# Kernel optimization log

Measured on AMD Instinct MI355X. Metric: run time of the kernel, lower is better.

## Reference

```python
import jax, jax.numpy as jnp
import numpy as np

N_NODES = 20000
N_EDGES = 320000
N_GRAPHS = 200
N_LAYERS = 2
TOWERS = 5
F_IN = 75        # divide_input=False -> each tower sees the full 75-dim input
F_OUT = 15       # out_channels // towers = 75 // 5
EDGE_DIM = 50
POST_IN = (4 * 3 + 1) * F_IN  # 4 aggregators * 3 scalers + self = 975
EPS_STD = 1e-5
EPS_BN = 1e-5


def setup_inputs() -> dict:
    key = jax.random.key(0)
    ks = jax.random.split(key, 16)
    x_idx = jax.random.randint(ks[0], (N_NODES,), 0, 10000)
    edge_index = jax.random.randint(ks[1], (2, N_EDGES), 0, N_NODES)
    edge_attr_idx = jax.random.randint(ks[2], (N_EDGES,), 0, 100)
    batch_idx = jnp.sort(jax.random.randint(ks[3], (N_NODES,), 0, N_GRAPHS))

    def g(k, shp, fan):
        return jax.random.normal(k, shp, jnp.float32) * np.float32(1.0 / np.sqrt(fan))

    inp = dict(
        x_idx=x_idx, edge_index=edge_index, edge_attr_idx=edge_attr_idx, batch_idx=batch_idx,
        node_emb=g(ks[4], (10000, F_IN), 1.0),
        edge_emb=g(ks[5], (100, EDGE_DIM), 1.0),
        W_edge=g(ks[6], (N_LAYERS, EDGE_DIM, F_IN), EDGE_DIM),
        b_edge=jnp.zeros((N_LAYERS, F_IN), jnp.float32),
        W_pre=g(ks[7], (N_LAYERS, TOWERS, 3 * F_IN, F_IN), 3 * F_IN),
        b_pre=jnp.zeros((N_LAYERS, TOWERS, F_IN), jnp.float32),
        W_post=g(ks[8], (N_LAYERS, TOWERS, POST_IN, F_OUT), POST_IN),
        b_post=jnp.zeros((N_LAYERS, TOWERS, F_OUT), jnp.float32),
        W_lin=g(ks[9], (N_LAYERS, F_IN, F_IN), F_IN),
        b_lin=jnp.zeros((N_LAYERS, F_IN), jnp.float32),
        bn_gamma=jnp.ones((N_LAYERS, F_IN), jnp.float32),
        bn_beta=jnp.zeros((N_LAYERS, F_IN), jnp.float32),
        W1=g(ks[10], (75, 50), 75), b1=jnp.zeros((50,), jnp.float32),
        W2=g(ks[11], (50, 25), 50), b2=jnp.zeros((25,), jnp.float32),
        W3=g(ks[12], (25, 1), 25), b3=jnp.zeros((1,), jnp.float32),
    )
    return inp


def reference(x_idx, edge_index, edge_attr_idx, batch_idx,
              node_emb, edge_emb, W_edge, b_edge, W_pre, b_pre,
              W_post, b_post, W_lin, b_lin, bn_gamma, bn_beta,
              W1, b1, W2, b2, W3, b3):
    src, dst = edge_index[0], edge_index[1]  # flow source_to_target: aggregate at dst
    x = node_emb[x_idx]                      # [N, 75]
    e_raw = edge_emb[edge_attr_idx]          # [E, 50]

    # in-degree based scalers (PNA); avg log-degree from this graph's degree histogram
    deg = jax.ops.segment_sum(jnp.ones((N_EDGES,), jnp.float32), dst, num_segments=N_NODES)
    avg_log = jnp.mean(jnp.log(deg + 1.0))
    deg_c = jnp.maximum(deg, 1.0)
    amp = (jnp.log(deg_c + 1.0) / avg_log)[:, None, None]
    att = (avg_log / jnp.log(deg_c + 1.0))[:, None, None]
    has_in = (deg > 0.0)[:, None, None]
    inv_deg = (1.0 / deg_c)[:, None, None]

    for l in range(N_LAYERS):
        # edge encoder (shared across towers)
        e = e_raw @ W_edge[l] + b_edge[l]                            # [E, 75]
        # message: since divide_input=False all towers see the same concat input
        h = jnp.concatenate([x[dst], x[src], e], axis=-1)            # [E, 225]
        m = jnp.einsum('ec,tcf->etf', h, W_pre[l]) + b_pre[l]        # [E, T, 75]
        # multi-aggregator reduction at dst
        mean = jax.ops.segment_sum(m, dst, num_segments=N_NODES) * inv_deg
        mean_sq = jax.ops.segment_sum(m * m, dst, num_segments=N_NODES) * inv_deg
        std = jnp.sqrt(jax.nn.relu(mean_sq - mean * mean) + EPS_STD)
        mn = jnp.where(has_in, jax.ops.segment_min(m, dst, num_segments=N_NODES), 0.0)
        mx = jnp.where(has_in, jax.ops.segment_max(m, dst, num_segments=N_NODES), 0.0)
        aggr = jnp.concatenate([mean, mn, mx, std], axis=-1)         # [N, T, 300]
        # degree scalers: identity, amplification, attenuation
        out = jnp.concatenate([aggr, aggr * amp, aggr * att], axis=-1)  # [N, T, 900]
        # update: concat self features, per-tower post MLP, then shared lin
        xt = jnp.broadcast_to(x[:, None, :], (N_NODES, TOWERS, F_IN))
        h2 = jnp.concatenate([xt, out], axis=-1)                     # [N, T, 975]
        y = jnp.einsum('ntc,tcf->ntf', h2, W_post[l]) + b_post[l]    # [N, T, 15]
        y = y.reshape(N_NODES, TOWERS * F_OUT) @ W_lin[l] + b_lin[l] # [N, 75]
        # BatchNorm (training-mode batch stats, biased variance) + ReLU
        mu = jnp.mean(y, axis=0)
        var = jnp.mean((y - mu) ** 2, axis=0)
        y = (y - mu) * jax.lax.rsqrt(var + EPS_BN) * bn_gamma[l] + bn_beta[l]
        x = jax.nn.relu(y)

    pooled = jax.ops.segment_sum(x, batch_idx, num_segments=N_GRAPHS)  # [G, 75]
    h = jax.nn.relu(pooled @ W1 + b1)
    h = jax.nn.relu(h @ W2 + b2)
    return h @ W3 + b3                                               # [G, 1]
```

## Files before the change

kernel.cpp:

```cpp
#include <hip/hip_runtime.h>
#include <hip/hip_bf16.h>
#include <math.h>

#define NN 20000
#define NE 320000
#define NG 200
#define FI 75
#define NT 5
#define FO 15
#define CH 375
#define PI 975

typedef __attribute__((ext_vector_type(8))) short v8s;
typedef __attribute__((ext_vector_type(4))) float v4f;

__device__ __forceinline__ unsigned short f2bfu(float v) {
  __hip_bfloat16 h = __float2bfloat16(v);
  return *reinterpret_cast<unsigned short*>(&h);
}
__device__ __forceinline__ float uif(unsigned u) { return __uint_as_float(u); }

__global__ __launch_bounds__(256) void k_mega1(
    const int* __restrict__ xidx, const float* __restrict__ emb, float* __restrict__ x,
    const int* __restrict__ dstp, int* __restrict__ deg,
    const float* __restrict__ eemb, const float* __restrict__ W_edge,
    const float* __restrict__ b_edge, float* __restrict__ te,
    const float* __restrict__ W_pre, float* __restrict__ WAs,
    const float* __restrict__ W_post, float* __restrict__ V,
    const float* __restrict__ b_post, const float* __restrict__ W_lin,
    const float* __restrict__ b_lin, float* __restrict__ bc) {
  __shared__ float S[FI * 16];
  int b = blockIdx.x, tid = threadIdx.x;
  if (b < 5860) {
    int i = b * 256 + tid;
    if (i < NN * FI) {
      int n = i / FI, f = i - n * FI;
      x[i] = emb[xidx[n] * FI + f];
    }
  } else if (b < 7110) {
    int e = (b - 5860) * 256 + tid;
    if (e < NE) atomicAdd(&deg[dstp[e]], 1);
  } else if (b < 7310) {
    int la = b - 7110;
    int l = la / 100, a = la - l * 100;
    int f = tid;
    if (f < FI) {
      float acc = b_edge[l * FI + f];
      for (int j = 0; j < 50; ++j)
        acc = fmaf(eemb[a * 50 + j], W_edge[(l * 50 + j) * FI + f], acc);
      te[la * FI + f] = acc;
    }
  } else if (b < 7530) {
    int i = (b - 7310) * 256 + tid;
    if (i < 2 * FI * CH) {
      int c = i % CH;
      int k = (i / CH) % FI;
      int l = i / (CH * FI);
      int t = c / FI, f = c - t * FI;
      WAs[i] = W_pre[((size_t)(l * NT + t) * 225 + FI + k) * FI + f];
    }
  } else if (b < 7560) {
    int bid = b - 7530;
    int g = bid % 3;
    int lt = bid / 3;
    for (int idx = tid; idx < FI * 16; idx += 256) {
      int q = idx >> 4, f = idx & 15;
      float v = 0.f;
      if (f < FO) {
        const float* wb = W_post + (size_t)lt * PI * FO;
        int rowb = FI + g * 300 + q;
        v = wb[rowb * FO + f] + wb[(rowb + FI) * FO + f] + wb[(rowb + 2 * FI) * FO + f];
      }
      S[idx] = v;
    }
    __syncthreads();
    for (int idx = tid; idx < FI * 16; idx += 256) {
      int j = idx >> 4, f = idx & 15;
      float acc = 0.f;
      const float* wr = W_pre + ((size_t)lt * 225 + j) * FI;
      for (int q = 0; q < FI; ++q) acc = fmaf(wr[q], S[q * 16 + f], acc);
      V[((size_t)bid * FI + j) * 16 + f] = acc;
    }
  } else {
    int l = b - 7560;
    int g = tid;
    if (g < FI) {
      float acc = b_lin[l * FI + g];
      for (int j = 0; j < FI; ++j)
        acc = fmaf(b_post[l * FI + j], W_lin[(l * FI + j) * FI + g], acc);
      bc[l * 76 + g] = acc;
    }
  }
}

__global__ __launch_bounds__(1024) void k_mega2(
    const int* __restrict__ deg, int* __restrict__ off, int* __restrict__ cur,
    float* __restrict__ avglog,
    const float* __restrict__ te, const float* __restrict__ W_pre,
    const float* __restrict__ b_pre, unsigned short* __restrict__ tm,
    const float* __restrict__ W_post, const float* __restrict__ V,
    unsigned short* __restrict__ Bp,
    const float* __restrict__ WAs, unsigned short* __restrict__ Bxs) {
  __shared__ float red[1024];
  int b = blockIdx.x, t = threadIdx.x;
  if (b == 0) {
    int* wsum = (int*)red;
    int base = t * 20;
    int loc[20];
    int s = 0;
#pragma unroll
    for (int j = 0; j < 20; ++j) {
      int i = base + j;
      int v = (i < NN) ? deg[i] : 0;
      loc[j] = s;
      s += v;
    }
    int lane = t & 63, w = t >> 6;
    int inc = s;
    for (int o = 1; o < 64; o <<= 1) {
      int u = __shfl_up(inc, o, 64);
      if (lane >= o) inc += u;
    }
    if (lane == 63) wsum[w] = inc;
    __syncthreads();
    if (t == 0) {
      int a = 0;
#pragma unroll
      for (int k = 0; k < 16; ++k) { int v = wsum[k]; wsum[k] = a; a += v; }
    }
    __syncthreads();
    int tex = wsum[w] + inc - s;
#pragma unroll
    for (int j = 0; j < 20; ++j) {
      int i = base + j;
      if (i < NN) { int e = tex + loc[j]; off[i] = e; cur[i] = e; }
    }
    if (t == 1023) off[NN] = tex + s;
  } else if (b == 1) {
    float s = 0.f;
    for (int i = t; i < NN; i += 1024) s += logf((float)deg[i] + 1.f);
    red[t] = s;
    __syncthreads();
    for (int o = 512; o > 0; o >>= 1) {
      if (t < o) red[t] += red[t + o];
      __syncthreads();
    }
    if (t == 0) avglog[0] = red[0] / (float)NN;
  } else if (b < 77) {
    int idx = (b - 2) * 1024 + t;
    if (idx < 76800) {
      int la = idx / 384, c = idx - la * 384;
      int l = la / 100;
      float acc = 0.f;
      if (c < CH) {
        int tt = c / FI, f = c - tt * FI;
        acc = b_pre[(l * NT + tt) * FI + f];
        const float* ter = te + la * FI;
        for (int k = 0; k < FI; ++k)
          acc = fmaf(ter[k], W_pre[((size_t)(l * NT + tt) * 225 + 150 + k) * FI + f], acc);
      }
      tm[(size_t)la * 384 + c] = f2bfu(acc);
    }
  } else if (b < 302) {
    int i = (b - 77) * 1024 + t;
    if (i < 230400) {
      int j = i & 7;
      int lane = (i >> 3) & 63;
      int rem = i >> 9;
      int kb = rem % 15; rem /= 15;
      int g = rem % 3; rem /= 3;
      int tt = rem % 5;
      int l = rem / 5;
      int k = kb * 32 + (lane >> 4) * 8 + j;
      int f = lane & 15;
      float w = 0.f;
      if (f < FO) {
        int lt = l * NT + tt;
        if (k < 300) {
          int a = k / 75, ch = k - a * 75;
          w = W_post[((size_t)lt * PI + FI + g * 300 + a * 75 + ch) * FO + f];
        } else if (k >= 320 && k < 395) {
          w = V[(((size_t)(lt * 3 + g)) * FI + (k - 320)) * 16 + f];
        } else if (k >= 395 && k < 470 && g == 0) {
          w = W_post[((size_t)lt * PI + (k - 395)) * FO + f];
        }
      }
      Bp[i] = f2bfu(w);
    }
  } else {
    int i = (b - 302) * 1024 + t;
    if (i < 73728) {
      int j = i & 7;
      int lane = (i >> 3) & 63;
      int rem = i >> 9;
      int nt = rem % 24; rem /= 24;
      int kb = rem % 3;
      int l = rem / 3;
      int k = kb * 32 + (lane >> 4) * 8 + j;
      int n = nt * 16 + (lane & 15);
      float w = 0.f;
      if (k < FI && n < CH) w = WAs[(size_t)l * FI * CH + k * CH + n];
      Bxs[i] = f2bfu(w);
    }
  }
}

__global__ __launch_bounds__(256) void k_mega3(
    const int* __restrict__ srcp, const int* __restrict__ dstp,
    const int* __restrict__ attr, int* __restrict__ cur, int2* __restrict__ csr,
    const int* __restrict__ deg, const float* __restrict__ avglog,
    float* __restrict__ amp, float* __restrict__ att, float* __restrict__ inv) {
  int b = blockIdx.x, t = threadIdx.x;
  if (b < 1250) {
    int e = b * 256 + t;
    if (e < NE) {
      int pos = atomicAdd(&cur[dstp[e]], 1);
      csr[pos] = make_int2(srcp[e], attr[e]);
    }
  } else {
    int i = (b - 1250) * 256 + t;
    if (i < NN) {
      float dc = fmaxf((float)deg[i], 1.f);
      float ld = logf(dc + 1.f);
      float av = avglog[0];
      amp[i] = ld / av;
      att[i] = av / ld;
      inv[i] = 1.f / dc;
    }
  }
}

__global__ __launch_bounds__(256) void k_gemm_xs(const float* __restrict__ x,
                                                 const unsigned short* __restrict__ BxsL,
                                                 unsigned short* __restrict__ xsb,
                                                 const int* __restrict__ deg,
                                                 unsigned short* __restrict__ xh,
                                                 float* __restrict__ bnsum) {
  int tid = threadIdx.x;
  if (blockIdx.y == 1) {
    if (blockIdx.x == 0 && tid < 150) bnsum[tid] = 0.f;
    for (int i = blockIdx.x * 256 + tid; i < NN * 160; i += 625 * 256) {
      int r = i / 160, k = i - r * 160;
      float v = 0.f;
      if (k < FI) v = x[(size_t)r * FI + k] * ((deg[r] > 0) ? 1.f : 0.f);
      else if (k < 150) v = x[(size_t)r * FI + k - FI];
      xh[i] = f2bfu(v);
    }
    return;
  }
  __shared__ unsigned short As[32 * 104];
  __shared__ unsigned short Os[32 * 384];
  int m0 = blockIdx.x * 32;
  for (int i = tid; i < 32 * 104; i += 256) {
    int r = i / 104, k = i - r * 104;
    As[i] = (k < FI) ? f2bfu(x[(size_t)(m0 + r) * FI + k]) : 0;
  }
  __syncthreads();
  int lane = tid & 63, w = tid >> 6;
  int m16 = lane & 15, quad = lane >> 4;
  v4f acc0[6], acc1[6];
#pragma unroll
  for (int nt = 0; nt < 6; ++nt) {
    acc0[nt] = {0.f, 0.f, 0.f, 0.f};
    acc1[nt] = {0.f, 0.f, 0.f, 0.f};
  }
  const unsigned short* arow0 = As + m16 * 104 + quad * 8;
  const unsigned short* arow1 = As + (16 + m16) * 104 + quad * 8;
#pragma unroll
  for (int kb = 0; kb < 3; ++kb) {
    v8s a0 = *(const v8s*)(arow0 + kb * 32);
    v8s a1 = *(const v8s*)(arow1 + kb * 32);
#pragma unroll
    for (int nt = 0; nt < 6; ++nt) {
      v8s bf = *(const v8s*)(BxsL + ((size_t)(kb * 24 + w * 6 + nt) * 64 + lane) * 8);
      acc0[nt] = __builtin_amdgcn_mfma_f32_16x16x32_bf16(a0, bf, acc0[nt], 0, 0, 0);
      acc1[nt] = __builtin_amdgcn_mfma_f32_16x16x32_bf16(a1, bf, acc1[nt], 0, 0, 0);
    }
  }
#pragma unroll
  for (int nt = 0; nt < 6; ++nt) {
    int col = w * 96 + nt * 16 + m16;
#pragma unroll
    for (int r = 0; r < 4; ++r) {
      Os[(quad * 4 + r) * 384 + col] = f2bfu(acc0[nt][r]);
      Os[(16 + quad * 4 + r) * 384 + col] = f2bfu(acc1[nt][r]);
    }
  }
  __syncthreads();
  uint4* dst = (uint4*)(xsb + (size_t)m0 * 384);
  const uint4* src = (const uint4*)Os;
  for (int i = tid; i < 1536; i += 256) dst[i] = src[i];
}

__global__ __launch_bounds__(192) void k_aggregate(int n0, int cn,
    const unsigned short* __restrict__ xs, const int2* __restrict__ csr,
    const int* __restrict__ off, const float* __restrict__ inv_deg,
    const unsigned short* __restrict__ tm, unsigned short* __restrict__ aggA) {
  __shared__ unsigned short sm[4 * 1600];
  int tid = threadIdx.x;
  int sub = tid / 48;
  int lane48 = tid - sub * 48;
  int rel0 = blockIdx.x * 4;
  int rel = rel0 + sub;
  for (int idx = tid; idx < 400; idx += 192) {
    int h = idx / 100, pp = idx - h * 100;
    int t = pp / 20, cc = pp - t * 20;
    sm[h * 1600 + t * 320 + 300 + cc] = 0;
  }
  if (rel < cn) {
    int n = n0 + rel;
    int c0 = lane48 * 8;
    int o0 = off[n], o1 = off[n + 1];
    float s[8], q[8], mn[8], mx[8];
#pragma unroll
    for (int j = 0; j < 8; ++j) {
      s[j] = 0.f; q[j] = 0.f; mn[j] = INFINITY; mx[j] = -INFINITY;
    }
    auto proc = [&](uint4 xv, uint4 tv) {
      unsigned xa[4] = {xv.x, xv.y, xv.z, xv.w};
      unsigned ta[4] = {tv.x, tv.y, tv.z, tv.w};
#pragma unroll
      for (int j = 0; j < 4; ++j) {
        float z0 = uif(xa[j] << 16) + uif(ta[j] << 16);
        float z1 = uif(xa[j] & 0xffff0000u) + uif(ta[j] & 0xffff0000u);
        s[2 * j] += z0; q[2 * j] = fmaf(z0, z0, q[2 * j]);
        mn[2 * j] = fminf(mn[2 * j], z0); mx[2 * j] = fmaxf(mx[2 * j], z0);
        s[2 * j + 1] += z1; q[2 * j + 1] = fmaf(z1, z1, q[2 * j + 1]);
        mn[2 * j + 1] = fminf(mn[2 * j + 1], z1); mx[2 * j + 1] = fmaxf(mx[2 * j + 1], z1);
      }
    };
    int i = o0;
    for (; i + 8 <= o1; i += 8) {
      int2 e0 = csr[i], e1 = csr[i + 1], e2 = csr[i + 2], e3 = csr[i + 3];
      int2 e4 = csr[i + 4], e5 = csr[i + 5], e6 = csr[i + 6], e7 = csr[i + 7];
      uint4 x0 = *(const uint4*)(xs + (size_t)e0.x * 384 + c0);
      uint4 t0 = *(const uint4*)(tm + (size_t)e0.y * 384 + c0);
      uint4 x1 = *(const uint4*)(xs + (size_t)e1.x * 384 + c0);
      uint4 t1 = *(const uint4*)(tm + (size_t)e1.y * 384 + c0);
      uint4 x2 = *(const uint4*)(xs + (size_t)e2.x * 384 + c0);
      uint4 t2 = *(const uint4*)(tm + (size_t)e2.y * 384 + c0);
      uint4 x3 = *(const uint4*)(xs + (size_t)e3.x * 384 + c0);
      uint4 t3 = *(const uint4*)(tm + (size_t)e3.y * 384 + c0);
      uint4 x4 = *(const uint4*)(xs + (size_t)e4.x * 384 + c0);
      uint4 t4 = *(const uint4*)(tm + (size_t)e4.y * 384 + c0);
      uint4 x5 = *(const uint4*)(xs + (size_t)e5.x * 384 + c0);
      uint4 t5 = *(const uint4*)(tm + (size_t)e5.y * 384 + c0);
      uint4 x6 = *(const uint4*)(xs + (size_t)e6.x * 384 + c0);
      uint4 t6 = *(const uint4*)(tm + (size_t)e6.y * 384 + c0);
      uint4 x7 = *(const uint4*)(xs + (size_t)e7.x * 384 + c0);
      uint4 t7 = *(const uint4*)(tm + (size_t)e7.y * 384 + c0);
      proc(x0, t0); proc(x1, t1); proc(x2, t2); proc(x3, t3);
      proc(x4, t4); proc(x5, t5); proc(x6, t6); proc(x7, t7);
    }
    for (; i + 2 <= o1; i += 2) {
      int2 e0 = csr[i], e1 = csr[i + 1];
      uint4 x0 = *(const uint4*)(xs + (size_t)e0.x * 384 + c0);
      uint4 t0 = *(const uint4*)(tm + (size_t)e0.y * 384 + c0);
      uint4 x1 = *(const uint4*)(xs + (size_t)e1.x * 384 + c0);
      uint4 t1 = *(const uint4*)(tm + (size_t)e1.y * 384 + c0);
      proc(x0, t0); proc(x1, t1);
    }
    if (i < o1) {
      int2 e0 = csr[i];
      uint4 x0 = *(const uint4*)(xs + (size_t)e0.x * 384 + c0);
      uint4 t0 = *(const uint4*)(tm + (size_t)e0.y * 384 + c0);
      proc(x0, t0);
    }
    float inv = inv_deg[n];
    bool empty = (o1 == o0);
    unsigned short* srow = sm + sub * 1600;
#pragma unroll
    for (int j = 0; j < 8; ++j) {
      int c = c0 + j;
      if (c < CH) {
        float me = s[j] * inv;
        float sd = sqrtf(fmaxf(q[j] * inv - me * me, 0.f) + 1e-5f);
        float mnv = empty ? 0.f : mn[j];
        float mxv = empty ? 0.f : mx[j];
        int t = c / 75, ch = c - t * 75;
        unsigned short* bb = srow + t * 320;
        bb[ch] = f2bfu(me);
        bb[75 + ch] = f2bfu(mnv);
        bb[150 + ch] = f2bfu(mxv);
        bb[225 + ch] = f2bfu(sd);
      }
    }
  }
  __syncthreads();
  int nrow = cn - rel0;
  if (nrow > 4) nrow = 4;
  if (nrow > 0) {
    int nu4 = nrow * 200;
    uint4* dst = (uint4*)(aggA + (size_t)rel0 * 1600);
    const uint4* src = (const uint4*)sm;
    for (int idx = tid; idx < nu4; idx += 192) dst[idx] = src[idx];
  }
}

__global__ __launch_bounds__(128) void k_mfma_post(int n0, int nend,
    const unsigned short* __restrict__ aggA, const unsigned short* __restrict__ xh,
    const unsigned short* __restrict__ Bp, const float* __restrict__ amp,
    const float* __restrict__ att, float* __restrict__ z) {
  int t = blockIdx.y;
  int lane = threadIdx.x & 63;
  int wv = threadIdx.x >> 6;
  int m16 = lane & 15, quad = lane >> 4;
  int relA = blockIdx.x * 32 + wv * 16 + m16;
  const unsigned short* arow = aggA + (size_t)relA * 1600 + t * 320 + quad * 8;
  const unsigned short* xrow = xh + (size_t)(n0 + relA) * 160 + quad * 8;
  const unsigned short* bp = Bp + ((size_t)t * 3 * 15 * 64) * 8 + lane * 8;
  v4f a0 = {0.f, 0.f, 0.f, 0.f}, a1 = a0, a2 = a0;
#pragma unroll
  for (int kb = 0; kb < 15; ++kb) {
    v8s av = *(const v8s*)((kb < 10) ? (arow + kb * 32) : (xrow + (kb - 10) * 32));
    const unsigned short* bb = bp + (size_t)kb * 512;
    v8s b0 = *(const v8s*)(bb);
    v8s b1 = *(const v8s*)(bb + 15 * 512);
    v8s b2 = *(const v8s*)(bb + 30 * 512);
    a0 = __builtin_amdgcn_mfma_f32_16x16x32_bf16(av, b0, a0, 0, 0, 0);
    a1 = __builtin_amdgcn_mfma_f32_16x16x32_bf16(av, b1, a1, 0, 0, 0);
    a2 = __builtin_amdgcn_mfma_f32_16x16x32_bf16(av, b2, a2, 0, 0, 0);
  }
  int f = m16;
  if (f < FO) {
    int relD0 = blockIdx.x * 32 + wv * 16 + quad * 4;
#pragma unroll
    for (int r = 0; r < 4; ++r) {
      int nd = n0 + relD0 + r;
      if (nd < nend) {
        float zz = a0[r] + amp[nd] * a1[r] + att[nd] * a2[r];
        z[(size_t)nd * FI + t * FO + f] = zz;
      }
    }
  }
}

__global__ __launch_bounds__(256) void k_gemm75(const float* __restrict__ zin,
    const float* __restrict__ Wl, const float* __restrict__ bcL,
    float* __restrict__ yout, float* __restrict__ bnsum) {
  __shared__ float Zs[64 * FI];
  __shared__ float Ws[FI * 76];
  __shared__ float ysum[FI], ysq[FI];
  int tid = threadIdx.x;
  int n0 = blockIdx.x * 64;
  for (int i = tid; i < 64 * FI; i += 256) {
    int n = n0 + i / FI;
    Zs[i] = (n < NN) ? zin[(size_t)n0 * FI + i] : 0.f;
  }
  for (int i = tid; i < FI * FI; i += 256) {
    int k = i / FI, f = i - k * FI;
    Ws[k * 76 + f] = Wl[i];
  }
  if (tid < FI) { ysum[tid] = 0.f; ysq[tid] = 0.f; }
  __syncthreads();
  int nl = tid >> 2, fg = tid & 3;
  int f0 = fg * 19;
  float acc[19];
#pragma unroll
  for (int i = 0; i < 19; ++i) acc[i] = bcL[f0 + i];
  for (int k = 0; k < FI; ++k) {
    float a = Zs[nl * FI + k];
#pragma unroll
    for (int i = 0; i < 19; ++i) acc[i] = fmaf(a, Ws[k * 76 + f0 + i], acc[i]);
  }
  int n = n0 + nl;
  if (n < NN) {
#pragma unroll
    for (int i = 0; i < 19; ++i) {
      int f = f0 + i;
      if (f < FI) {
        float v = acc[i];
        yout[(size_t)n * FI + f] = v;
        atomicAdd(&ysum[f], v);
        atomicAdd(&ysq[f], v * v);
      }
    }
  }
  __syncthreads();
  if (tid < FI) {
    atomicAdd(&bnsum[tid], ysum[tid]);
    atomicAdd(&bnsum[FI + tid], ysq[tid]);
  }
}

__global__ __launch_bounds__(256) void k_bnfinapply(const float* __restrict__ y,
    const float* __restrict__ bnsum, const float* __restrict__ gamL,
    const float* __restrict__ betL, float* __restrict__ xo,
    const int* __restrict__ batch, float* __restrict__ pooled, int dopool) {
  __shared__ float sc[150];
  int tid = threadIdx.x;
  if (tid < FI) {
    float mu = bnsum[tid] / (float)NN;
    float var = bnsum[FI + tid] / (float)NN - mu * mu;
    float scl = gamL[tid] * rsqrtf(var + 1e-5f);
    sc[tid] = scl;
    sc[FI + tid] = betL[tid] - mu * scl;
  }
  if (!dopool) {
    for (int i = blockIdx.x * 256 + tid; i < NG * FI; i += gridDim.x * 256)
      pooled[i] = 0.f;
  }
  __syncthreads();
  int stride = gridDim.x * 256;
  for (int i = blockIdx.x * 256 + tid; i < NN * FI; i += stride) {
    int n = i / FI, f = i - n * FI;
    float v = fmaxf(fmaf(y[i], sc[f], sc[FI + f]), 0.f);
    xo[i] = v;
    if (dopool) atomicAdd(&pooled[batch[n] * FI + f], v);
  }
}

__global__ void k_head(const float* __restrict__ pooled, const float* __restrict__ W1,
                       const float* __restrict__ b1, const float* __restrict__ W2,
                       const float* __restrict__ b2, const float* __restrict__ W3,
                       const float* __restrict__ b3, float* __restrict__ out) {
  __shared__ float p[FI], h1[50], h2[25];
  int g = blockIdx.x, t = threadIdx.x;
  for (int i = t; i < FI; i += 64) p[i] = pooled[g * FI + i];
  __syncthreads();
  if (t < 50) {
    float a = b1[t];
    for (int j = 0; j < FI; ++j) a = fmaf(p[j], W1[j * 50 + t], a);
    h1[t] = fmaxf(a, 0.f);
  }
  __syncthreads();
  if (t < 25) {
    float a = b2[t];
    for (int j = 0; j < 50; ++j) a = fmaf(h1[j], W2[j * 25 + t], a);
    h2[t] = fmaxf(a, 0.f);
  }
  __syncthreads();
  if (t == 0) {
    float a = b3[0];
    for (int j = 0; j < 25; ++j) a = fmaf(h2[j], W3[j], a);
    out[g] = a;
  }
}

extern "C" void kernel_launch(void* const* d_in, const int* in_sizes, int n_in,
                              void* d_out, int out_size, void* d_ws, size_t ws_size,
                              hipStream_t stream) {
  const int* x_idx = (const int*)d_in[0];
  const int* eidx  = (const int*)d_in[1];
  const int* srcp  = eidx;
  const int* dstp  = eidx + NE;
  const int* eattr = (const int*)d_in[2];
  const int* batch = (const int*)d_in[3];
  const float* node_emb = (const float*)d_in[4];
  const float* edge_emb = (const float*)d_in[5];
  const float* W_edge = (const float*)d_in[6];
  const float* b_edge = (const float*)d_in[7];
  const float* W_pre  = (const float*)d_in[8];
  const float* b_pre  = (const float*)d_in[9];
  const float* W_post = (const float*)d_in[10];
  const float* b_post = (const float*)d_in[11];
  const float* W_lin  = (const float*)d_in[12];
  const float* b_lin  = (const float*)d_in[13];
  const float* gam = (const float*)d_in[14];
  const float* bet = (const float*)d_in[15];
  const float* W1 = (const float*)d_in[16];
  const float* b1 = (const float*)d_in[17];
  const float* W2 = (const float*)d_in[18];
  const float* b2 = (const float*)d_in[19];
  const float* W3 = (const float*)d_in[20];
  const float* b3 = (const float*)d_in[21];

  char* p = (char*)d_ws;
  auto alloc = [&](size_t b) -> char* {
    char* r = p;
    p += (b + 255) & ~(size_t)255;
    return r;
  };
  float* x_a   = (float*)alloc((size_t)NN * FI * 4);
  float* x_b   = (float*)alloc((size_t)NN * FI * 4);
  unsigned short* xs_bf = (unsigned short*)alloc((size_t)NN * 384 * 2);
  float* z     = (float*)alloc((size_t)NN * FI * 4);
  unsigned short* xh = (unsigned short*)alloc((size_t)(NN + 32) * 160 * 2);
  float* te    = (float*)alloc(2 * 100 * FI * 4);
  unsigned short* tm_bf = (unsigned short*)alloc((size_t)2 * 100 * 384 * 2);
  float* WAs   = (float*)alloc((size_t)2 * FI * CH * 4);
  float* V     = (float*)alloc((size_t)2 * NT * 3 * FI * 16 * 4);
  unsigned short* Bpk = (unsigned short*)alloc((size_t)230400 * 2);
  unsigned short* Bxs = (unsigned short*)alloc((size_t)73728 * 2);
  float* bc    = (float*)alloc(2 * 76 * 4);
  float* ampv  = (float*)alloc((size_t)NN * 4);
  float* attv  = (float*)alloc((size_t)NN * 4);
  float* invv  = (float*)alloc((size_t)NN * 4);
  float* avglog = (float*)alloc(256);
  float* bnsum = (float*)alloc(2 * FI * 4);
  float* pooled = (float*)alloc((size_t)NG * FI * 4);
  int* deg = (int*)alloc((size_t)NN * 4);
  int* off = (int*)alloc((size_t)(NN + 1) * 4);
  int* cur = (int*)alloc((size_t)NN * 4);
  int2* csr = (int2*)alloc((size_t)NE * 8);
  size_t used = (size_t)(p - (char*)d_ws);
  int chunkN = NN;
  while (chunkN > 2500 &&
         used + (size_t)((chunkN + 31) & ~31) * 1600 * 2 + (1 << 20) > ws_size)
    chunkN >>= 1;
  int rows = (chunkN + 31) & ~31;
  unsigned short* aggA = (unsigned short*)alloc((size_t)rows * 1600 * 2);

  hipMemsetAsync(deg, 0, (size_t)NN * 4, stream);

  k_mega1<<<7562, 256, 0, stream>>>(x_idx, node_emb, x_a, dstp, deg,
                                    edge_emb, W_edge, b_edge, te,
                                    W_pre, WAs, W_post, V,
                                    b_post, W_lin, b_lin, bc);
  k_mega2<<<374, 1024, 0, stream>>>(deg, off, cur, avglog,
                                    te, W_pre, b_pre, tm_bf, W_post, V, Bpk,
                                    WAs, Bxs);
  k_mega3<<<1329, 256, 0, stream>>>(srcp, dstp, eattr, cur, csr,
                                    deg, avglog, ampv, attv, invv);

  for (int l = 0; l < 2; ++l) {
    const float* xin = (l == 0) ? x_a : x_b;
    float* xout = (l == 0) ? x_b : x_a;
    k_gemm_xs<<<dim3(625, 2), 256, 0, stream>>>(xin, Bxs + (size_t)l * 36864,
                                                xs_bf, deg, xh, bnsum);
    for (int n0 = 0; n0 < NN; n0 += chunkN) {
      int cn = (NN - n0 < chunkN) ? (NN - n0) : chunkN;
      k_aggregate<<<(cn + 3) / 4, 192, 0, stream>>>(n0, cn, xs_bf, csr, off, invv,
                                                    tm_bf + (size_t)l * 100 * 384, aggA);
      k_mfma_post<<<dim3((cn + 31) / 32, 5), 128, 0, stream>>>(
          n0, n0 + cn, aggA, xh, Bpk + (size_t)l * 115200, ampv, attv, z);
    }
    k_gemm75<<<313, 256, 0, stream>>>(z, W_lin + (size_t)l * FI * FI, bc + l * 76,
                                      z, bnsum);
    k_bnfinapply<<<1250, 256, 0, stream>>>(z, bnsum, gam + l * FI, bet + l * FI,
                                           xout, batch, pooled, (l == 1) ? 1 : 0);
  }

  k_head<<<NG, 64, 0, stream>>>(pooled, W1, b1, W2, b2, W3, b3, (float*)d_out);
}
```

Measured before the change: 490.8 us.

## Process nodes in descending-degree order via counting-sort permutation for load balance

```diff
diff --git a/kernel.cpp b/kernel.cpp
--- a/kernel.cpp
+++ b/kernel.cpp
@@ -28,7 +28,8 @@
     const float* __restrict__ W_pre, float* __restrict__ WAs,
     const float* __restrict__ W_post, float* __restrict__ V,
     const float* __restrict__ b_post, const float* __restrict__ W_lin,
-    const float* __restrict__ b_lin, float* __restrict__ bc) {
+    const float* __restrict__ b_lin, float* __restrict__ bc,
+    int* __restrict__ hist) {
   __shared__ float S[FI * 16];
   int b = blockIdx.x, tid = threadIdx.x;
   if (b < 5860) {
@@ -81,7 +82,7 @@
       for (int q = 0; q < FI; ++q) acc = fmaf(wr[q], S[q * 16 + f], acc);
       V[((size_t)bid * FI + j) * 16 + f] = acc;
     }
-  } else {
+  } else if (b < 7562) {
     int l = b - 7560;
     int g = tid;
     if (g < FI) {
@@ -90,6 +91,8 @@
         acc = fmaf(b_post[l * FI + j], W_lin[(l * FI + j) * FI + g], acc);
       bc[l * 76 + g] = acc;
     }
+  } else {
+    for (int i = tid; i < 1024; i += 256) hist[i] = 0;
   }
 }
 
@@ -100,7 +103,8 @@
     const float* __restrict__ b_pre, unsigned short* __restrict__ tm,
     const float* __restrict__ W_post, const float* __restrict__ V,
     unsigned short* __restrict__ Bp,
-    const float* __restrict__ WAs, unsigned short* __restrict__ Bxs) {
+    const float* __restrict__ WAs, unsigned short* __restrict__ Bxs,
+    int* __restrict__ hist) {
   __shared__ float red[1024];
   int b = blockIdx.x, t = threadIdx.x;
   if (b == 0) {
@@ -187,7 +191,7 @@
       }
       Bp[i] = f2bfu(w);
     }
-  } else {
+  } else if (b < 374) {
     int i = (b - 302) * 1024 + t;
     if (i < 73728) {
       int j = i & 7;
@@ -202,6 +206,43 @@
       if (k < FI && n < CH) w = WAs[(size_t)l * FI * CH + k * CH + n];
       Bxs[i] = f2bfu(w);
     }
+  } else {
+    int i = (b - 374) * 1024 + t;
+    if (i < NN) {
+      int d = deg[i];
+      if (d > 1023) d = 1023;
+      atomicAdd(&hist[1023 - d], 1);
+    }
+  }
+}
+
+__global__ __launch_bounds__(1024) void k_scanperm(const int* __restrict__ deg,
+                                                   int* __restrict__ hist,
+                                                   int* __restrict__ perm) {
+  __shared__ int ws[16];
+  int t = threadIdx.x;
+  int v = hist[t];
+  int lane = t & 63, w = t >> 6;
+  int inc = v;
+  for (int o = 1; o < 64; o <<= 1) {
+    int u = __shfl_up(inc, o, 64);
+    if (lane >= o) inc += u;
+  }
+  if (lane == 63) ws[w] = inc;
+  __syncthreads();
+  if (t == 0) {
+    int a = 0;
+#pragma unroll
+    for (int k = 0; k < 16; ++k) { int x = ws[k]; ws[k] = a; a += x; }
+  }
+  __syncthreads();
+  hist[t] = ws[w] + inc - v;
+  __syncthreads();
+  for (int n = t; n < NN; n += 1024) {
+    int d = deg[n];
+    if (d > 1023) d = 1023;
+    int pos = atomicAdd(&hist[1023 - d], 1);
+    perm[pos] = n;
   }
 }
 
@@ -295,7 +336,8 @@
 __global__ __launch_bounds__(192) void k_aggregate(int n0, int cn,
     const unsigned short* __restrict__ xs, const int2* __restrict__ csr,
     const int* __restrict__ off, const float* __restrict__ inv_deg,
-    const unsigned short* __restrict__ tm, unsigned short* __restrict__ aggA) {
+    const unsigned short* __restrict__ tm, unsigned short* __restrict__ aggA,
+    const int* __restrict__ perm) {
   __shared__ unsigned short sm[4 * 1600];
   int tid = threadIdx.x;
   int sub = tid / 48;
@@ -308,7 +350,7 @@
     sm[h * 1600 + t * 320 + 300 + cc] = 0;
   }
   if (rel < cn) {
-    int n = n0 + rel;
+    int n = perm[n0 + rel];
     int c0 = lane48 * 8;
     int o0 = off[n], o1 = off[n + 1];
     float s[8], q[8], mn[8], mx[8];
@@ -400,14 +442,18 @@
 __global__ __launch_bounds__(128) void k_mfma_post(int n0, int nend,
     const unsigned short* __restrict__ aggA, const unsigned short* __restrict__ xh,
     const unsigned short* __restrict__ Bp, const float* __restrict__ amp,
-    const float* __restrict__ att, float* __restrict__ z) {
+    const float* __restrict__ att, float* __restrict__ z,
+    const int* __restrict__ perm) {
   int t = blockIdx.y;
   int lane = threadIdx.x & 63;
   int wv = threadIdx.x >> 6;
   int m16 = lane & 15, quad = lane >> 4;
   int relA = blockIdx.x * 32 + wv * 16 + m16;
+  int idxA = n0 + relA;
+  if (idxA >= NN) idxA = NN - 1;
+  int ndA = perm[idxA];
   const unsigned short* arow = aggA + (size_t)relA * 1600 + t * 320 + quad * 8;
-  const unsigned short* xrow = xh + (size_t)(n0 + relA) * 160 + quad * 8;
+  const unsigned short* xrow = xh + (size_t)ndA * 160 + quad * 8;
   const unsigned short* bp = Bp + ((size_t)t * 3 * 15 * 64) * 8 + lane * 8;
   v4f a0 = {0.f, 0.f, 0.f, 0.f}, a1 = a0, a2 = a0;
 #pragma unroll
@@ -426,8 +472,9 @@
     int relD0 = blockIdx.x * 32 + wv * 16 + quad * 4;
 #pragma unroll
     for (int r = 0; r < 4; ++r) {
-      int nd = n0 + relD0 + r;
-      if (nd < nend) {
+      int slot = n0 + relD0 + r;
+      if (slot < nend) {
+        int nd = perm[slot];
         float zz = a0[r] + amp[nd] * a1[r] + att[nd] * a2[r];
         z[(size_t)nd * FI + t * FO + f] = zz;
       }
@@ -592,6 +639,8 @@
   int* deg = (int*)alloc((size_t)NN * 4);
   int* off = (int*)alloc((size_t)(NN + 1) * 4);
   int* cur = (int*)alloc((size_t)NN * 4);
+  int* hist = (int*)alloc(1024 * 4);
+  int* perm = (int*)alloc((size_t)NN * 4);
   int2* csr = (int2*)alloc((size_t)NE * 8);
   size_t used = (size_t)(p - (char*)d_ws);
   int chunkN = NN;
@@ -603,13 +652,14 @@
 
   hipMemsetAsync(deg, 0, (size_t)NN * 4, stream);
 
-  k_mega1<<<7562, 256, 0, stream>>>(x_idx, node_emb, x_a, dstp, deg,
+  k_mega1<<<7563, 256, 0, stream>>>(x_idx, node_emb, x_a, dstp, deg,
                                     edge_emb, W_edge, b_edge, te,
                                     W_pre, WAs, W_post, V,
-                                    b_post, W_lin, b_lin, bc);
-  k_mega2<<<374, 1024, 0, stream>>>(deg, off, cur, avglog,
+                                    b_post, W_lin, b_lin, bc, hist);
+  k_mega2<<<394, 1024, 0, stream>>>(deg, off, cur, avglog,
                                     te, W_pre, b_pre, tm_bf, W_post, V, Bpk,
-                                    WAs, Bxs);
+                                    WAs, Bxs, hist);
+  k_scanperm<<<1, 1024, 0, stream>>>(deg, hist, perm);
   k_mega3<<<1329, 256, 0, stream>>>(srcp, dstp, eattr, cur, csr,
                                     deg, avglog, ampv, attv, invv);
 
@@ -621,9 +671,10 @@
     for (int n0 = 0; n0 < NN; n0 += chunkN) {
       int cn = (NN - n0 < chunkN) ? (NN - n0) : chunkN;
       k_aggregate<<<(cn + 3) / 4, 192, 0, stream>>>(n0, cn, xs_bf, csr, off, invv,
-                                                    tm_bf + (size_t)l * 100 * 384, aggA);
+                                                    tm_bf + (size_t)l * 100 * 384, aggA,
+                                                    perm);
       k_mfma_post<<<dim3((cn + 31) / 32, 5), 128, 0, stream>>>(
-          n0, n0 + cn, aggA, xh, Bpk + (size_t)l * 115200, ampv, attv, z);
+          n0, n0 + cn, aggA, xh, Bpk + (size_t)l * 115200, ampv, attv, z, perm);
     }
     k_gemm75<<<313, 256, 0, stream>>>(z, W_lin + (size_t)l * FI * FI, bc + l * 76,
                                       z, bnsum);
```

Measured after the change: 648.1 us. 32.0% more time.

## Fuse per-tower MFMA post projection with shared 75x75 linear and BN stats

Applied to the files above, without the earlier changes.

```diff
diff --git a/kernel.cpp b/kernel.cpp
--- a/kernel.cpp
+++ b/kernel.cpp
@@ -397,74 +397,67 @@
   }
 }
 
-__global__ __launch_bounds__(128) void k_mfma_post(int n0, int nend,
+__global__ __launch_bounds__(128) void k_post2(int n0, int nend,
     const unsigned short* __restrict__ aggA, const unsigned short* __restrict__ xh,
     const unsigned short* __restrict__ Bp, const float* __restrict__ amp,
-    const float* __restrict__ att, float* __restrict__ z) {
-  int t = blockIdx.y;
-  int lane = threadIdx.x & 63;
-  int wv = threadIdx.x >> 6;
-  int m16 = lane & 15, quad = lane >> 4;
-  int relA = blockIdx.x * 32 + wv * 16 + m16;
-  const unsigned short* arow = aggA + (size_t)relA * 1600 + t * 320 + quad * 8;
-  const unsigned short* xrow = xh + (size_t)(n0 + relA) * 160 + quad * 8;
-  const unsigned short* bp = Bp + ((size_t)t * 3 * 15 * 64) * 8 + lane * 8;
-  v4f a0 = {0.f, 0.f, 0.f, 0.f}, a1 = a0, a2 = a0;
-#pragma unroll
-  for (int kb = 0; kb < 15; ++kb) {
-    v8s av = *(const v8s*)((kb < 10) ? (arow + kb * 32) : (xrow + (kb - 10) * 32));
-    const unsigned short* bb = bp + (size_t)kb * 512;
-    v8s b0 = *(const v8s*)(bb);
-    v8s b1 = *(const v8s*)(bb + 15 * 512);
-    v8s b2 = *(const v8s*)(bb + 30 * 512);
-    a0 = __builtin_amdgcn_mfma_f32_16x16x32_bf16(av, b0, a0, 0, 0, 0);
-    a1 = __builtin_amdgcn_mfma_f32_16x16x32_bf16(av, b1, a1, 0, 0, 0);
-    a2 = __builtin_amdgcn_mfma_f32_16x16x32_bf16(av, b2, a2, 0, 0, 0);
-  }
-  int f = m16;
-  if (f < FO) {
-    int relD0 = blockIdx.x * 32 + wv * 16 + quad * 4;
-#pragma unroll
-    for (int r = 0; r < 4; ++r) {
-      int nd = n0 + relD0 + r;
-      if (nd < nend) {
-        float zz = a0[r] + amp[nd] * a1[r] + att[nd] * a2[r];
-        z[(size_t)nd * FI + t * FO + f] = zz;
-      }
-    }
-  }
-}
-
-__global__ __launch_bounds__(256) void k_gemm75(const float* __restrict__ zin,
-    const float* __restrict__ Wl, const float* __restrict__ bcL,
-    float* __restrict__ yout, float* __restrict__ bnsum) {
-  __shared__ float Zs[64 * FI];
+    const float* __restrict__ att, const float* __restrict__ Wl,
+    const float* __restrict__ bcL, float* __restrict__ yout,
+    float* __restrict__ bnsum) {
+  __shared__ float zs[32][76];
   __shared__ float Ws[FI * 76];
   __shared__ float ysum[FI], ysq[FI];
   int tid = threadIdx.x;
-  int n0 = blockIdx.x * 64;
-  for (int i = tid; i < 64 * FI; i += 256) {
-    int n = n0 + i / FI;
-    Zs[i] = (n < NN) ? zin[(size_t)n0 * FI + i] : 0.f;
-  }
-  for (int i = tid; i < FI * FI; i += 256) {
+  for (int i = tid; i < FI * FI; i += 128) {
     int k = i / FI, f = i - k * FI;
     Ws[k * 76 + f] = Wl[i];
   }
   if (tid < FI) { ysum[tid] = 0.f; ysq[tid] = 0.f; }
+  int lane = tid & 63, wv = tid >> 6;
+  int m16 = lane & 15, quad = lane >> 4;
+  int relA = blockIdx.x * 32 + wv * 16 + m16;
+  const unsigned short* arow = aggA + (size_t)relA * 1600 + quad * 8;
+  const unsigned short* xrow = xh + (size_t)(n0 + relA) * 160 + quad * 8;
+  for (int t = 0; t < NT; ++t) {
+    const unsigned short* bp = Bp + ((size_t)t * 3 * 15 * 64) * 8 + lane * 8;
+    v4f a0 = {0.f, 0.f, 0.f, 0.f}, a1 = a0, a2 = a0;
+#pragma unroll
+    for (int kb = 0; kb < 15; ++kb) {
+      v8s av = *(const v8s*)((kb < 10) ? (arow + t * 320 + kb * 32)
+                                       : (xrow + (kb - 10) * 32));
+      const unsigned short* bb = bp + (size_t)kb * 512;
+      v8s b0 = *(const v8s*)(bb);
+      v8s b1 = *(const v8s*)(bb + 15 * 512);
+      v8s b2 = *(const v8s*)(bb + 30 * 512);
+      a0 = __builtin_amdgcn_mfma_f32_16x16x32_bf16(av, b0, a0, 0, 0, 0);
+      a1 = __builtin_amdgcn_mfma_f32_16x16x32_bf16(av, b1, a1, 0, 0, 0);
+      a2 = __builtin_amdgcn_mfma_f32_16x16x32_bf16(av, b2, a2, 0, 0, 0);
+    }
+    int f = m16;
+    if (f < FO) {
+      int relD0 = wv * 16 + quad * 4;
+#pragma unroll
+      for (int r = 0; r < 4; ++r) {
+        int nd = n0 + blockIdx.x * 32 + relD0 + r;
+        if (nd < nend) {
+          float zz = a0[r] + amp[nd] * a1[r] + att[nd] * a2[r];
+          zs[relD0 + r][t * FO + f] = zz;
+        }
+      }
+    }
+  }
   __syncthreads();
   int nl = tid >> 2, fg = tid & 3;
   int f0 = fg * 19;
-  float acc[19];
-#pragma unroll
-  for (int i = 0; i < 19; ++i) acc[i] = bcL[f0 + i];
-  for (int k = 0; k < FI; ++k) {
-    float a = Zs[nl * FI + k];
-#pragma unroll
-    for (int i = 0; i < 19; ++i) acc[i] = fmaf(a, Ws[k * 76 + f0 + i], acc[i]);
-  }
-  int n = n0 + nl;
-  if (n < NN) {
+  int n = n0 + blockIdx.x * 32 + nl;
+  if (n < nend) {
+    float acc[19];
+#pragma unroll
+    for (int i = 0; i < 19; ++i) acc[i] = bcL[f0 + i];
+    for (int k = 0; k < FI; ++k) {
+      float a = zs[nl][k];
+#pragma unroll
+      for (int i = 0; i < 19; ++i) acc[i] = fmaf(a, Ws[k * 76 + f0 + i], acc[i]);
+    }
 #pragma unroll
     for (int i = 0; i < 19; ++i) {
       int f = f0 + i;
@@ -622,11 +615,10 @@
       int cn = (NN - n0 < chunkN) ? (NN - n0) : chunkN;
       k_aggregate<<<(cn + 3) / 4, 192, 0, stream>>>(n0, cn, xs_bf, csr, off, invv,
                                                     tm_bf + (size_t)l * 100 * 384, aggA);
-      k_mfma_post<<<dim3((cn + 31) / 32, 5), 128, 0, stream>>>(
-          n0, n0 + cn, aggA, xh, Bpk + (size_t)l * 115200, ampv, attv, z);
-    }
-    k_gemm75<<<313, 256, 0, stream>>>(z, W_lin + (size_t)l * FI * FI, bc + l * 76,
-                                      z, bnsum);
+      k_post2<<<(cn + 31) / 32, 128, 0, stream>>>(
+          n0, n0 + cn, aggA, xh, Bpk + (size_t)l * 115200, ampv, attv,
+          W_lin + (size_t)l * FI * FI, bc + l * 76, z, bnsum);
+    }
     k_bnfinapply<<<1250, 256, 0, stream>>>(z, bnsum, gam + l * FI, bet + l * FI,
                                            xout, batch, pooled, (l == 1) ? 1 : 0);
   }
```

After: 471.9 us. -3.9%, faster.
